# Kernel optimization log

Measured on AMD Instinct MI355X. Metric: run time of the kernel, lower is better.

## Reference

```python
import math
import jax, jax.numpy as jnp
import numpy as np

V, D_S, D_F, N_PASSES, N_HEADS, MAX_LEN, FFN_MULT = 32000, 128, 1024, 3, 4, 2048, 4
B, L = 2, 2048


def _ln(x, g, b, eps=1e-5):
    m = x.mean(-1, keepdims=True)
    v = ((x - m) ** 2).mean(-1, keepdims=True)
    return (x - m) * jax.lax.rsqrt(v + eps) * g + b


def _pairwise_kernel(q, mu, log_var, tau):
    # M[t,j] = q_t^2 . iv_j - 2 q_t . (mu_j*iv_j) + mu_j^2 . iv_j  -> [B,L,L]
    iv = jnp.exp(-log_var)
    mu_iv = mu * iv
    mu2_iv_sum = (mu * mu_iv).sum(-1)                      # [B,L]
    term1 = jnp.einsum('btd,bjd->btj', q * q, iv)
    term2 = jnp.einsum('btd,bjd->btj', q, mu_iv)
    mahal = term1 - 2.0 * term2 + mu2_iv_sum[:, None, :]
    return jnp.exp(-0.5 * mahal / tau)


def _causal_render(features, alpha, K, causal_mask):
    eff_a = alpha[:, None, :] * K * causal_mask            # [B,L,L]
    eff_a = jnp.clip(eff_a, 0.0, 1.0 - 1e-6)
    log_1ma = jnp.log1p(-eff_a)
    log_cum = jnp.cumsum(log_1ma, axis=-1)
    log_T = jnp.concatenate([jnp.zeros_like(log_cum[:, :, :1]), log_cum[:, :, :-1]], axis=-1)
    weights = eff_a * jnp.exp(log_T)
    return jnp.einsum('btj,bjf->btf', weights, features)


def setup_inputs() -> dict:
    key = jax.random.key(0)
    ks = jax.random.split(key, 16)
    P = N_PASSES - 1
    n = lambda k, shape, std: jax.random.normal(k, shape, dtype=jnp.float32) * std
    inp = {
        'token_ids': jax.random.randint(ks[0], (B, L), 0, V),
        'tok_mu': n(ks[1], (V, D_S), 0.02),
        'tok_log_var': jnp.zeros((V, D_S), jnp.float32),
        'tok_raw_alpha': jnp.zeros((V, 1), jnp.float32),
        'tok_features': n(ks[2], (V, D_F), 0.02),
        'pos_mu': n(ks[3], (MAX_LEN, D_S), 0.01),
        'log_tau': jnp.asarray(math.log(128.0), jnp.float32),
        'qp_w': jnp.broadcast_to(jnp.eye(D_S, dtype=jnp.float32), (N_HEADS, D_S, D_S)).copy(),
        'qp_b': jnp.zeros((N_HEADS, D_S), jnp.float32),
        'hp_w': n(ks[4], (D_F, N_HEADS * D_F), 0.02 / math.sqrt(2 * N_PASSES)),
        'hp_b': jnp.zeros((D_F,), jnp.float32),
        'mu_w': n(ks[5], (P, D_S, 2 * D_F), 0.02),
        'mu_b': jnp.zeros((P, D_S), jnp.float32),
        'ag_w': n(ks[6], (P, 1, 2 * D_F), 0.02),
        'ag_b': jnp.zeros((P, 1), jnp.float32),
        'ffn_ln_g': jnp.ones((P, 2 * D_F), jnp.float32),
        'ffn_ln_b': jnp.zeros((P, 2 * D_F), jnp.float32),
        'ffn_w1': n(ks[7], (P, FFN_MULT * D_F, 2 * D_F), 0.02),
        'ffn_b1': jnp.zeros((P, FFN_MULT * D_F), jnp.float32),
        'ffn_w2': n(ks[8], (P, D_F, FFN_MULT * D_F), 0.02),
        'ffn_b2': jnp.zeros((P, D_F), jnp.float32),
        'lnf_g': jnp.ones((D_F,), jnp.float32),
        'lnf_b': jnp.zeros((D_F,), jnp.float32),
        'lm_w': n(ks[9], (V, D_F), 0.02),
    }
    return inp


def reference(token_ids, tok_mu, tok_log_var, tok_raw_alpha, tok_features, pos_mu,
              log_tau, qp_w, qp_b, hp_w, hp_b, mu_w, mu_b, ag_w, ag_b,
              ffn_ln_g, ffn_ln_b, ffn_w1, ffn_b1, ffn_w2, ffn_b2, lnf_g, lnf_b, lm_w):
    Bsz, Ln = token_ids.shape
    mu = tok_mu[token_ids] + pos_mu[:Ln][None]             # [B,L,d_s]
    log_var = tok_log_var[token_ids]
    alpha = jax.nn.sigmoid(tok_raw_alpha[token_ids][..., 0])  # [B,L]
    features = tok_features[token_ids]                     # [B,L,d_f]
    tau = jnp.exp(log_tau)
    causal_mask = jnp.tril(jnp.ones((Ln, Ln), jnp.float32))
    meaning = None
    for p in range(N_PASSES):
        head_meanings = []
        for h in range(N_HEADS):
            q_h = jnp.einsum('bld,ed->ble', mu, qp_w[h]) + qp_b[h]
            K_h = _pairwise_kernel(q_h, mu, log_var, tau)
            head_meanings.append(_causal_render(features, alpha, K_h, causal_mask))
        meaning = jnp.einsum('blc,fc->blf', jnp.concatenate(head_meanings, -1), hp_w) + hp_b
        if p < N_PASSES - 1:
            ctx = jnp.concatenate([features, meaning], -1)  # [B,L,2*d_f]
            mu = mu + jnp.tanh(jnp.einsum('blc,dc->bld', ctx, mu_w[p]) + mu_b[p])
            alpha = alpha * jax.nn.sigmoid(jnp.einsum('blc,oc->blo', ctx, ag_w[p]) + ag_b[p])[..., 0]
            h1 = _ln(ctx, ffn_ln_g[p], ffn_ln_b[p])
            h2 = jax.nn.gelu(jnp.einsum('blc,hc->blh', h1, ffn_w1[p]) + ffn_b1[p], approximate=False)
            features = features + jnp.einsum('blh,fh->blf', h2, ffn_w2[p]) + ffn_b2[p]
    logits = jnp.einsum('blf,vf->blv', _ln(meaning, lnf_g, lnf_b), lm_w)
    return logits
```

## Files before the change

### kernel.cpp

```cpp
#include <hip/hip_runtime.h>

#define BB 2
#define LL 2048
#define DS 128
#define DF 1024
#define NH 4
#define NP 3
#define VV 32000
#define FFH 4096
#define CTXD 2048
#define RR (BB*LL)
#define NHDF (NH*DF)

enum { EPI_NONE=0, EPI_TANH=1, EPI_GELU=2, EPI_EXPM=3 };

#define BM 128
#define BN 128
#define BK 8

template<int EPI, bool BETA, bool BT, bool TRI>
__global__ __launch_bounds__(256) void gemm_f32(
    const float* __restrict__ A, int lda, long sA,
    const float* __restrict__ B, int ldb, long sB,
    float* __restrict__ C, int ldc, long sC,
    int M, int N, int K,
    const float* __restrict__ bias,
    const float* __restrict__ m2s, long sM2,
    const float* __restrict__ log_tau)
{
    __shared__ __align__(16) float As[BK][BM];
    __shared__ __align__(16) float Bs[BK][BN];
    int z = blockIdx.z;
    A += (long)z * sA; B += (long)z * sB; C += (long)z * sC;
    const float* m2p = (EPI == EPI_EXPM) ? (m2s + (long)z * sM2) : nullptr;

    int m0 = blockIdx.y * BM;
    int n0 = blockIdx.x * BN;
    int tid = threadIdx.x;
    int tx = tid & 15, ty = tid >> 4;

    float acc[8][8];
    #pragma unroll
    for (int i = 0; i < 8; i++)
        #pragma unroll
        for (int j = 0; j < 8; j++) acc[i][j] = 0.f;

    int kEnd = K;
    if (TRI) { int km = m0 + BM; kEnd = km < K ? km : K; }

    int arow = tid >> 1, akk = (tid & 1) * 4;
    for (int k0 = 0; k0 < kEnd; k0 += BK) {
        float4 av = *(const float4*)(A + (long)(m0 + arow) * lda + k0 + akk);
        As[akk+0][arow] = av.x; As[akk+1][arow] = av.y;
        As[akk+2][arow] = av.z; As[akk+3][arow] = av.w;
        if (BT) {
            float4 bv = *(const float4*)(B + (long)(n0 + arow) * ldb + k0 + akk);
            Bs[akk+0][arow] = bv.x; Bs[akk+1][arow] = bv.y;
            Bs[akk+2][arow] = bv.z; Bs[akk+3][arow] = bv.w;
        } else {
            int brow = tid >> 5, bcol = (tid & 31) * 4;
            float4 bv = *(const float4*)(B + (long)(k0 + brow) * ldb + n0 + bcol);
            *(float4*)&Bs[brow][bcol] = bv;
        }
        __syncthreads();
        #pragma unroll
        for (int kk = 0; kk < BK; kk++) {
            float a[8], b[8];
            *(float4*)&a[0] = *(const float4*)&As[kk][ty*8];
            *(float4*)&a[4] = *(const float4*)&As[kk][ty*8+4];
            *(float4*)&b[0] = *(const float4*)&Bs[kk][tx*8];
            *(float4*)&b[4] = *(const float4*)&Bs[kk][tx*8+4];
            #pragma unroll
            for (int i = 0; i < 8; i++)
                #pragma unroll
                for (int j = 0; j < 8; j++)
                    acc[i][j] = fmaf(a[i], b[j], acc[i][j]);
        }
        __syncthreads();
    }

    float scale = 0.f;
    if (EPI == EPI_EXPM) scale = -0.5f * expf(-log_tau[0]);

    #pragma unroll
    for (int i = 0; i < 8; i++) {
        int row = m0 + ty*8 + i;
        float* cp = C + (long)row * ldc + n0 + tx*8;
        float out[8];
        #pragma unroll
        for (int j = 0; j < 8; j++) {
            float v = acc[i][j];
            int col = n0 + tx*8 + j;
            if (EPI == EPI_EXPM) {
                v = expf(scale * (v + m2p[col]));
            } else {
                if (bias) v += bias[col];
                if (EPI == EPI_TANH) v = tanhf(v);
                else if (EPI == EPI_GELU) v = 0.5f*v*(1.f + erff(v*0.70710678118654752f));
            }
            out[j] = v;
        }
        if (BETA) {
            float4 c0 = *(const float4*)(cp);
            float4 c1 = *(const float4*)(cp + 4);
            out[0]+=c0.x; out[1]+=c0.y; out[2]+=c0.z; out[3]+=c0.w;
            out[4]+=c1.x; out[5]+=c1.y; out[6]+=c1.z; out[7]+=c1.w;
        }
        *(float4*)cp       = make_float4(out[0],out[1],out[2],out[3]);
        *(float4*)(cp + 4) = make_float4(out[4],out[5],out[6],out[7]);
    }
}

__global__ __launch_bounds__(256) void embed_kernel(
    const int* __restrict__ ids, const float* __restrict__ tok_mu,
    const float* __restrict__ tok_lv, const float* __restrict__ tok_ra,
    const float* __restrict__ tok_f, const float* __restrict__ pos_mu,
    float* __restrict__ mu, float* __restrict__ iv,
    float* __restrict__ alpha, float* __restrict__ feat)
{
    int r = blockIdx.x; int l = r % LL;
    int id = ids[r];
    int tid = threadIdx.x;
    for (int i = tid; i < DS; i += 256) {
        mu[(long)r*DS + i] = tok_mu[(long)id*DS + i] + pos_mu[(long)l*DS + i];
        iv[(long)r*DS + i] = expf(-tok_lv[(long)id*DS + i]);
    }
    for (int i = tid; i < DF; i += 256)
        feat[(long)r*DF + i] = tok_f[(long)id*DF + i];
    if (tid == 0) alpha[r] = 1.f/(1.f + expf(-tok_ra[id]));
}

__global__ __launch_bounds__(256) void alpha_kernel(
    const float* __restrict__ ctx, const float* __restrict__ agw,
    const float* __restrict__ agb, float* __restrict__ alpha)
{
    int r = blockIdx.x;
    const float* xr = ctx + (long)r*CTXD;
    __shared__ float red[256];
    int tid = threadIdx.x;
    float s = 0.f;
    for (int i = tid; i < CTXD; i += 256) s += xr[i]*agw[i];
    red[tid] = s; __syncthreads();
    for (int st = 128; st > 0; st >>= 1) { if (tid < st) red[tid] += red[tid+st]; __syncthreads(); }
    if (tid == 0) alpha[r] *= 1.f/(1.f + expf(-(red[0] + agb[0])));
}

__global__ __launch_bounds__(256) void ctx_kernel(
    const float* __restrict__ feat, const float* __restrict__ meaning, float* __restrict__ ctx)
{
    long i4 = (long)blockIdx.x * 256 + threadIdx.x;
    long r = i4 >> 9;
    long c4 = i4 & 511;
    const float4* src = (c4 < 256) ? (const float4*)(feat + r*DF) + c4
                                   : (const float4*)(meaning + r*DF) + (c4 - 256);
    ((float4*)ctx)[i4] = *src;
}

__global__ __launch_bounds__(128) void qbuild_kernel(
    const float* __restrict__ mu, const float* __restrict__ iv,
    float* __restrict__ Q, float* __restrict__ m2s)
{
    int r = blockIdx.x; int d = threadIdx.x;
    float ivd = iv[(long)r*DS + d];
    float m   = mu[(long)r*DS + d];
    Q[(long)r*256 + d]       = ivd;
    Q[(long)r*256 + 128 + d] = m * ivd;
    __shared__ float red[128];
    red[d] = m*m*ivd; __syncthreads();
    for (int s = 64; s > 0; s >>= 1) { if (d < s) red[d] += red[d+s]; __syncthreads(); }
    if (d == 0) m2s[r] = red[0];
}

__global__ __launch_bounds__(128) void pbuild_kernel(const float* __restrict__ q, float* __restrict__ P)
{
    int r = blockIdx.x; int d = threadIdx.x;
    float qv = q[(long)r*DS + d];
    P[(long)r*256 + d]       = qv*qv;
    P[(long)r*256 + 128 + d] = -2.f*qv;
}

__global__ __launch_bounds__(256) void scan_weights(float* __restrict__ Kmat, const float* __restrict__ alpha)
{
    int r = blockIdx.x;
    int b = r / LL, t = r % LL;
    float* row = Kmat + (long)r * LL;
    const float* al = alpha + (long)b * LL;
    int tid = threadIdx.x;
    int lane = tid & 63, wid = tid >> 6;
    __shared__ float wtot[4];
    float carry = 1.f;
    for (int j0 = 0; j0 < LL; j0 += 256) {
        int j = j0 + tid;
        if (j0 > t) { row[j] = 0.f; continue; }
        float eff = 0.f;
        if (j <= t) eff = fminf(al[j] * row[j], 1.f - 1e-6f);
        float om = 1.f - eff;
        float incl = om;
        #pragma unroll
        for (int d = 1; d < 64; d <<= 1) {
            float v = __shfl_up(incl, d);
            if (lane >= d) incl *= v;
        }
        if (lane == 63) wtot[wid] = incl;
        float excl = __shfl_up(incl, 1);
        if (lane == 0) excl = 1.f;
        __syncthreads();
        float wpre = carry;
        for (int w = 0; w < wid; w++) wpre *= wtot[w];
        row[j] = eff * wpre * excl;
        float tot = wtot[0]*wtot[1]*wtot[2]*wtot[3];
        __syncthreads();
        carry *= tot;
    }
}

template<int C>
__global__ __launch_bounds__(256) void ln_kernel(
    const float* __restrict__ x, const float* __restrict__ g,
    const float* __restrict__ b, float* __restrict__ y)
{
    int r = blockIdx.x;
    const float* xr = x + (long)r*C;
    __shared__ float xs[C];
    __shared__ float red[256];
    int tid = threadIdx.x;
    float s = 0.f;
    for (int i = tid; i < C; i += 256) { float v = xr[i]; xs[i] = v; s += v; }
    red[tid] = s; __syncthreads();
    for (int st = 128; st > 0; st >>= 1) { if (tid < st) red[tid] += red[tid+st]; __syncthreads(); }
    float mean = red[0] / C;
    __syncthreads();
    float s2 = 0.f;
    for (int i = tid; i < C; i += 256) { float d = xs[i]-mean; s2 += d*d; }
    red[tid] = s2; __syncthreads();
    for (int st = 128; st > 0; st >>= 1) { if (tid < st) red[tid] += red[tid+st]; __syncthreads(); }
    float rs = rsqrtf(red[0]/C + 1e-5f);
    for (int i = tid; i < C; i += 256) y[(long)r*C + i] = (xs[i]-mean)*rs*g[i] + b[i];
}

typedef __attribute__((ext_vector_type(8))) short bf8;
typedef __attribute__((ext_vector_type(4))) float f4;

__device__ __forceinline__ unsigned short bf16_rne(float x){
    unsigned u = __builtin_bit_cast(unsigned, x);
    u += 0x7FFFu + ((u >> 16) & 1u);
    return (unsigned short)(u >> 16);
}
__device__ __forceinline__ float bf16f(unsigned short h){
    unsigned u = ((unsigned)h) << 16;
    return __builtin_bit_cast(float, u);
}
__device__ __forceinline__ void split2(float x, unsigned short& h, unsigned short& l){
    h = bf16_rne(x);
    l = bf16_rne(x - bf16f(h));
}
__device__ __forceinline__ f4 mfma_b(bf8 a, bf8 b, f4 c){
    return __builtin_amdgcn_mfma_f32_16x16x32_bf16(a, b, c, 0, 0, 0);
}

template<int EPI, bool BETA, bool TRI, bool OSPLIT>
__global__ __launch_bounds__(256, 2) void gemm_mf(
    const unsigned short* __restrict__ Ah, const unsigned short* __restrict__ Al, int lda, long sA,
    const unsigned short* __restrict__ Bh, const unsigned short* __restrict__ Bl, int ldb, long sB,
    float* __restrict__ C, unsigned short* __restrict__ Ch, unsigned short* __restrict__ Cl,
    int ldc, long sC, int M, int N, int K,
    const float* __restrict__ bias, const float* __restrict__ m2s, long sM2,
    const float* __restrict__ log_tau)
{
    __shared__ __align__(16) unsigned short lds[4][4][128][8];

    int z = blockIdx.z;
    Ah += (long)z * sA; Al += (long)z * sA;
    Bh += (long)z * sB; Bl += (long)z * sB;
    if (OSPLIT) { Ch += (long)z * sC; Cl += (long)z * sC; }
    else        { C  += (long)z * sC; }
    const float* m2p = (EPI == EPI_EXPM) ? (m2s + (long)z * sM2) : nullptr;

    int m0 = blockIdx.y * 128, n0 = blockIdx.x * 128;
    int tid  = threadIdx.x;
    int lane = tid & 63, wave = tid >> 6;
    int wm = wave >> 1, wn = wave & 1;
    int kc = lane >> 4, lr = lane & 15;

    f4 acc[4][4];
    #pragma unroll
    for (int i = 0; i < 4; i++)
        #pragma unroll
        for (int j = 0; j < 4; j++)
            #pragma unroll
            for (int r = 0; r < 4; r++) acc[i][j][r] = 0.f;

    int kEnd = K;
    if (TRI) { int km = m0 + 128; kEnd = km < K ? km : K; }

    int s0 = tid, s1 = tid + 256;
    int row0 = s0 & 127, c0 = s0 >> 7;
    int row1 = s1 & 127, c1 = s1 >> 7;

    for (int kt = 0; kt < kEnd; kt += 32) {
        long a0 = (long)(m0 + row0) * lda + kt + c0 * 8;
        long a1 = (long)(m0 + row1) * lda + kt + c1 * 8;
        long b0 = (long)(n0 + row0) * ldb + kt + c0 * 8;
        long b1 = (long)(n0 + row1) * ldb + kt + c1 * 8;
        uint4 vah0 = *(const uint4*)(Ah + a0);
        uint4 vah1 = *(const uint4*)(Ah + a1);
        uint4 val0 = *(const uint4*)(Al + a0);
        uint4 val1 = *(const uint4*)(Al + a1);
        uint4 vbh0 = *(const uint4*)(Bh + b0);
        uint4 vbh1 = *(const uint4*)(Bh + b1);
        uint4 vbl0 = *(const uint4*)(Bl + b0);
        uint4 vbl1 = *(const uint4*)(Bl + b1);
        *(uint4*)&lds[0][c0][row0][0] = vah0;
        *(uint4*)&lds[0][c1][row1][0] = vah1;
        *(uint4*)&lds[1][c0][row0][0] = val0;
        *(uint4*)&lds[1][c1][row1][0] = val1;
        *(uint4*)&lds[2][c0][row0][0] = vbh0;
        *(uint4*)&lds[2][c1][row1][0] = vbh1;
        *(uint4*)&lds[3][c0][row0][0] = vbl0;
        *(uint4*)&lds[3][c1][row1][0] = vbl1;
        __syncthreads();

        bf8 ah[4], al4[4], bh4[4], bl4[4];
        #pragma unroll
        for (int i = 0; i < 4; i++) {
            ah[i]  = *(const bf8*)&lds[0][kc][wm*64 + i*16 + lr][0];
            al4[i] = *(const bf8*)&lds[1][kc][wm*64 + i*16 + lr][0];
            bh4[i] = *(const bf8*)&lds[2][kc][wn*64 + i*16 + lr][0];
            bl4[i] = *(const bf8*)&lds[3][kc][wn*64 + i*16 + lr][0];
        }
        #pragma unroll
        for (int i = 0; i < 4; i++)
            #pragma unroll
            for (int j = 0; j < 4; j++) {
                acc[i][j] = mfma_b(ah[i],  bh4[j], acc[i][j]);
                acc[i][j] = mfma_b(al4[i], bh4[j], acc[i][j]);
                acc[i][j] = mfma_b(ah[i],  bl4[j], acc[i][j]);
            }
        __syncthreads();
    }

    float scale = 0.f;
    if (EPI == EPI_EXPM) scale = -0.5f * expf(-log_tau[0]);
    int r0 = (lane >> 4) * 4;
    #pragma unroll
    for (int i = 0; i < 4; i++) {
        int rowb = m0 + wm*64 + i*16 + r0;
        #pragma unroll
        for (int j = 0; j < 4; j++) {
            int col = n0 + wn*64 + j*16 + lr;
            float bv = 0.f, m2v = 0.f;
            if (EPI == EPI_EXPM) m2v = m2p[col];
            else if (bias) bv = bias[col];
            #pragma unroll
            for (int r = 0; r < 4; r++) {
                long off = (long)(rowb + r) * ldc + col;
                float v = acc[i][j][r];
                if (EPI == EPI_EXPM) v = expf(scale * (v + m2v));
                else {
                    v += bv;
                    if (EPI == EPI_TANH) v = tanhf(v);
                    else if (EPI == EPI_GELU) v = 0.5f*v*(1.f + erff(v*0.70710678118654752f));
                }
                if (OSPLIT) {
                    unsigned short hh, llo; split2(v, hh, llo);
                    Ch[off] = hh; Cl[off] = llo;
                } else {
                    if (BETA) v += C[off];
                    C[off] = v;
                }
            }
        }
    }
}

__global__ __launch_bounds__(256) void split_kernel(
    const float* __restrict__ x, unsigned short* __restrict__ h, unsigned short* __restrict__ l)
{
    long i = (long)blockIdx.x * 256 + threadIdx.x;
    float4 v = ((const float4*)x)[i];
    ushort4 hv, lv;
    split2(v.x, hv.x, lv.x); split2(v.y, hv.y, lv.y);
    split2(v.z, hv.z, lv.z); split2(v.w, hv.w, lv.w);
    ((ushort4*)h)[i] = hv;
    ((ushort4*)l)[i] = lv;
}

__global__ __launch_bounds__(256) void tsplit_kernel(
    const float* __restrict__ x, unsigned short* __restrict__ th, unsigned short* __restrict__ tl)
{
    __shared__ float t[32][33];
    int bx = blockIdx.x, by = blockIdx.y;
    int tx = threadIdx.x & 31, ty = threadIdx.x >> 5;
    #pragma unroll
    for (int k = 0; k < 4; k++)
        t[ty + 8*k][tx] = x[(long)(by*32 + ty + 8*k)*DF + bx*32 + tx];
    __syncthreads();
    #pragma unroll
    for (int k = 0; k < 4; k++) {
        float v = t[tx][ty + 8*k];
        unsigned short hh, llo; split2(v, hh, llo);
        long o = (long)(bx*32 + ty + 8*k)*RR + by*32 + tx;
        th[o] = hh; tl[o] = llo;
    }
}

__global__ __launch_bounds__(128) void qbuild_mf(
    const float* __restrict__ mu, const float* __restrict__ iv,
    unsigned short* __restrict__ Qh, unsigned short* __restrict__ Ql,
    float* __restrict__ m2s)
{
    int r = blockIdx.x; int d = threadIdx.x;
    float ivd = iv[(long)r*DS + d];
    float m   = mu[(long)r*DS + d];
    unsigned short hh, llo;
    split2(ivd, hh, llo);
    Qh[(long)r*256 + d] = hh;        Ql[(long)r*256 + d] = llo;
    split2(m * ivd, hh, llo);
    Qh[(long)r*256 + 128 + d] = hh;  Ql[(long)r*256 + 128 + d] = llo;
    __shared__ float red[128];
    red[d] = m*m*ivd; __syncthreads();
    for (int s = 64; s > 0; s >>= 1) { if (d < s) red[d] += red[d+s]; __syncthreads(); }
    if (d == 0) m2s[r] = red[0];
}

__global__ __launch_bounds__(128) void pbuild_mf(
    const float* __restrict__ q,
    unsigned short* __restrict__ Ph, unsigned short* __restrict__ Pl)
{
    int r = blockIdx.x; int d = threadIdx.x;
    float qv = q[(long)r*DS + d];
    unsigned short hh, llo;
    split2(qv*qv, hh, llo);
    Ph[(long)r*256 + d] = hh;        Pl[(long)r*256 + d] = llo;
    split2(-2.f*qv, hh, llo);
    Ph[(long)r*256 + 128 + d] = hh;  Pl[(long)r*256 + 128 + d] = llo;
}

__global__ __launch_bounds__(256) void scan_weights_mf(
    const float* __restrict__ Kmat, const float* __restrict__ alpha,
    unsigned short* __restrict__ Wh, unsigned short* __restrict__ Wl)
{
    int r = blockIdx.x;
    int b = r / LL, t = r % LL;
    const float* row = Kmat + (long)r * LL;
    unsigned short* wh = Wh + (long)r * LL;
    unsigned short* wl = Wl + (long)r * LL;
    const float* al = alpha + (long)b * LL;
    int tid = threadIdx.x;
    int lane = tid & 63, wid = tid >> 6;
    __shared__ float wtot[4];
    float carry = 1.f;
    for (int j0 = 0; j0 < LL; j0 += 256) {
        int j = j0 + tid;
        if (j0 > t) { wh[j] = 0; wl[j] = 0; continue; }
        float eff = 0.f;
        if (j <= t) eff = fminf(al[j] * row[j], 1.f - 1e-6f);
        float om = 1.f - eff;
        float incl = om;
        #pragma unroll
        for (int d = 1; d < 64; d <<= 1) {
            float v = __shfl_up(incl, d);
            if (lane >= d) incl *= v;
        }
        if (lane == 63) wtot[wid] = incl;
        float excl = __shfl_up(incl, 1);
        if (lane == 0) excl = 1.f;
        __syncthreads();
        float wpre = carry;
        for (int w = 0; w < wid; w++) wpre *= wtot[w];
        float val = eff * wpre * excl;
        unsigned short hh, llo; split2(val, hh, llo);
        wh[j] = hh; wl[j] = llo;
        float tot = wtot[0]*wtot[1]*wtot[2]*wtot[3];
        __syncthreads();
        carry *= tot;
    }
}

template<int C>
__global__ __launch_bounds__(256) void ln_mf(
    const float* __restrict__ x, const float* __restrict__ g,
    const float* __restrict__ b, unsigned short* __restrict__ yh, unsigned short* __restrict__ yl)
{
    int r = blockIdx.x;
    const float* xr = x + (long)r*C;
    __shared__ float xs[C];
    __shared__ float red[256];
    int tid = threadIdx.x;
    float s = 0.f;
    for (int i = tid; i < C; i += 256) { float v = xr[i]; xs[i] = v; s += v; }
    red[tid] = s; __syncthreads();
    for (int st = 128; st > 0; st >>= 1) { if (tid < st) red[tid] += red[tid+st]; __syncthreads(); }
    float mean = red[0] / C;
    __syncthreads();
    float s2 = 0.f;
    for (int i = tid; i < C; i += 256) { float d = xs[i]-mean; s2 += d*d; }
    red[tid] = s2; __syncthreads();
    for (int st = 128; st > 0; st >>= 1) { if (tid < st) red[tid] += red[tid+st]; __syncthreads(); }
    float rs = rsqrtf(red[0]/C + 1e-5f);
    for (int i = tid; i < C; i += 256) {
        float v = (xs[i]-mean)*rs*g[i] + b[i];
        unsigned short hh, llo; split2(v, hh, llo);
        yh[(long)r*C + i] = hh; yl[(long)r*C + i] = llo;
    }
}

static void launch_legacy(void* const* d_in, void* d_out, void* d_ws, hipStream_t stream)
{
    const int*   token_ids = (const int*)d_in[0];
    const float* tok_mu  = (const float*)d_in[1];
    const float* tok_lv  = (const float*)d_in[2];
    const float* tok_ra  = (const float*)d_in[3];
    const float* tok_f   = (const float*)d_in[4];
    const float* pos_mu  = (const float*)d_in[5];
    const float* log_tau = (const float*)d_in[6];
    const float* qp_w = (const float*)d_in[7];
    const float* qp_b = (const float*)d_in[8];
    const float* hp_w = (const float*)d_in[9];
    const float* hp_b = (const float*)d_in[10];
    const float* mu_w = (const float*)d_in[11];
    const float* mu_b = (const float*)d_in[12];
    const float* ag_w = (const float*)d_in[13];
    const float* ag_b = (const float*)d_in[14];
    const float* ln_g = (const float*)d_in[15];
    const float* ln_b = (const float*)d_in[16];
    const float* w1 = (const float*)d_in[17];
    const float* b1 = (const float*)d_in[18];
    const float* w2 = (const float*)d_in[19];
    const float* b2 = (const float*)d_in[20];
    const float* lnf_g = (const float*)d_in[21];
    const float* lnf_b = (const float*)d_in[22];
    const float* lm_w  = (const float*)d_in[23];
    float* out = (float*)d_out;

    float* ws      = (float*)d_ws;
    float* mu      = ws;
    float* iv      = mu + 524288;
    float* alpha   = iv + 524288;
    float* m2s     = alpha + 4096;
    float* q       = m2s + 4096;
    float* P       = q + 524288;
    float* Q       = P + 1048576;
    float* feat    = Q + 1048576;
    float* meaning = feat + 4194304;
    float* head_m  = meaning + 4194304;
    float* ctx     = head_m + 4194304;
    float* Kbuf    = ctx + 8388608;
    float* h1  = Kbuf;
    float* h2  = head_m;
    float* lnm = head_m;

    const int R = BB * LL;

    embed_kernel<<<R, 256, 0, stream>>>(token_ids, tok_mu, tok_lv, tok_ra, tok_f, pos_mu,
                                        mu, iv, alpha, feat);

    for (int p = 0; p < NP; p++) {
        qbuild_kernel<<<R, 128, 0, stream>>>(mu, iv, Q, m2s);
        for (int h = 0; h < NH; h++) {
            dim3 g1(DS/BN, R/BM, 1);
            gemm_f32<EPI_NONE,false,true,false><<<g1,256,0,stream>>>(
                mu, DS, 0, qp_w + (long)h*DS*DS, DS, 0, q, DS, 0,
                R, DS, DS, qp_b + h*DS, nullptr, 0, nullptr);
            pbuild_kernel<<<R, 128, 0, stream>>>(q, P);
            dim3 g2(LL/BN, LL/BM, BB);
            gemm_f32<EPI_EXPM,false,true,false><<<g2,256,0,stream>>>(
                P, 256, (long)LL*256, Q, 256, (long)LL*256, Kbuf, LL, (long)LL*LL,
                LL, LL, 256, nullptr, m2s, LL, log_tau);
            scan_weights<<<R, 256, 0, stream>>>(Kbuf, alpha);
            dim3 g3(DF/BN, LL/BM, BB);
            gemm_f32<EPI_NONE,false,false,true><<<g3,256,0,stream>>>(
                Kbuf, LL, (long)LL*LL, feat, DF, (long)LL*DF, head_m, DF, (long)LL*DF,
                LL, DF, LL, nullptr, nullptr, 0, nullptr);
            dim3 g4(DF/BN, R/BM, 1);
            if (h == 0)
                gemm_f32<EPI_NONE,false,true,false><<<g4,256,0,stream>>>(
                    head_m, DF, 0, hp_w + (long)h*DF, NH*DF, 0, meaning, DF, 0,
                    R, DF, DF, hp_b, nullptr, 0, nullptr);
            else
                gemm_f32<EPI_NONE,true,true,false><<<g4,256,0,stream>>>(
                    head_m, DF, 0, hp_w + (long)h*DF, NH*DF, 0, meaning, DF, 0,
                    R, DF, DF, nullptr, nullptr, 0, nullptr);
        }
        if (p < NP - 1) {
            ctx_kernel<<<(R*CTXD/4)/256, 256, 0, stream>>>(feat, meaning, ctx);
            dim3 g5(DS/BN, R/BM, 1);
            gemm_f32<EPI_TANH,true,true,false><<<g5,256,0,stream>>>(
                ctx, CTXD, 0, mu_w + (long)p*DS*CTXD, CTXD, 0, mu, DS, 0,
                R, DS, CTXD, mu_b + p*DS, nullptr, 0, nullptr);
            alpha_kernel<<<R, 256, 0, stream>>>(ctx, ag_w + (long)p*CTXD, ag_b + p, alpha);
            ln_kernel<CTXD><<<R, 256, 0, stream>>>(ctx, ln_g + (long)p*CTXD, ln_b + (long)p*CTXD, h1);
            for (int c = 0; c < 4; c++) {
                long ro = (long)c * 1024;
                dim3 g6(FFH/BN, 1024/BM, 1);
                gemm_f32<EPI_GELU,false,true,false><<<g6,256,0,stream>>>(
                    h1 + ro*CTXD, CTXD, 0, w1 + (long)p*FFH*CTXD, CTXD, 0, h2, FFH, 0,
                    1024, FFH, CTXD, b1 + (long)p*FFH, nullptr, 0, nullptr);
                dim3 g7(DF/BN, 1024/BM, 1);
                gemm_f32<EPI_NONE,true,true,false><<<g7,256,0,stream>>>(
                    h2, FFH, 0, w2 + (long)p*DF*FFH, FFH, 0, feat + ro*DF, DF, 0,
                    1024, DF, FFH, b2 + (long)p*DF, nullptr, 0, nullptr);
            }
        }
    }

    ln_kernel<DF><<<R, 256, 0, stream>>>(meaning, lnf_g, lnf_b, lnm);
    dim3 g8(VV/BN, R/BM, 1);
    gemm_f32<EPI_NONE,false,true,false><<<g8,256,0,stream>>>(
        lnm, DF, 0, lm_w, DF, 0, out, VV, 0,
        R, VV, DF, nullptr, nullptr, 0, nullptr);
}

extern "C" void kernel_launch(void* const* d_in, const int* in_sizes, int n_in,
                              void* d_out, int out_size, void* d_ws, size_t ws_size,
                              hipStream_t stream)
{
    const size_t WS_NEED = 174096384;
    if (ws_size < WS_NEED) {
        launch_legacy(d_in, d_out, d_ws, stream);
        return;
    }

    const int*   token_ids = (const int*)d_in[0];
    const float* tok_mu  = (const float*)d_in[1];
    const float* tok_lv  = (const float*)d_in[2];
    const float* tok_ra  = (const float*)d_in[3];
    const float* tok_f   = (const float*)d_in[4];
    const float* pos_mu  = (const float*)d_in[5];
    const float* log_tau = (const float*)d_in[6];
    const float* qp_w = (const float*)d_in[7];
    const float* qp_b = (const float*)d_in[8];
    const float* hp_w = (const float*)d_in[9];
    const float* hp_b = (const float*)d_in[10];
    const float* mu_w = (const float*)d_in[11];
    const float* mu_b = (const float*)d_in[12];
    const float* ag_w = (const float*)d_in[13];
    const float* ag_b = (const float*)d_in[14];
    const float* ln_g = (const float*)d_in[15];
    const float* ln_b = (const float*)d_in[16];
    const float* w1 = (const float*)d_in[17];
    const float* b1 = (const float*)d_in[18];
    const float* w2 = (const float*)d_in[19];
    const float* b2 = (const float*)d_in[20];
    const float* lnf_g = (const float*)d_in[21];
    const float* lnf_b = (const float*)d_in[22];
    const float* lm_w  = (const float*)d_in[23];
    float* out = (float*)d_out;

    float* ws      = (float*)d_ws;
    float* mu      = ws;
    float* iv      = mu + 524288;
    float* alpha   = iv + 524288;
    float* m2s     = alpha + 4096;
    float* q       = m2s + 4096;
    float* feat    = q + 524288;
    float* meaning = feat + 4194304;
    float* ctxK    = meaning + 4194304;
    float* Kbuf = ctxK;
    float* ctx  = ctxK;

    unsigned short* pool = (unsigned short*)(ctxK + 8388608);
    unsigned short* featT_h = pool;
    unsigned short* featT_l = pool + 4194304;
    unsigned short* hpw_h   = pool + 8388608;
    unsigned short* hpw_l   = pool + 12582912;
    unsigned short* P_h     = pool + 16777216;
    unsigned short* P_l     = pool + 17825792;
    unsigned short* Q_h     = pool + 18874368;
    unsigned short* Q_l     = pool + 19922944;
    unsigned short* W_h     = pool + 20971520;
    unsigned short* W_l     = pool + 29360128;
    unsigned short* hm_h    = pool + 37748736;
    unsigned short* hm_l    = pool + 41943040;
    unsigned short* h1_h  = pool;
    unsigned short* h1_l  = pool + 4194304;
    unsigned short* w1s_h = pool + 8388608;
    unsigned short* w1s_l = pool + 16777216;
    unsigned short* h2_h  = pool + 25165824;
    unsigned short* h2_l  = pool + 33554432;
    unsigned short* w2s_h = pool + 41943040;
    unsigned short* w2s_l = pool + 46137344;
    unsigned short* lnm_h = pool;
    unsigned short* lnm_l = pool + 4194304;
    unsigned short* lmw_h = pool + 8388608;
    unsigned short* lmw_l = pool + 24772608;

    embed_kernel<<<RR, 256, 0, stream>>>(token_ids, tok_mu, tok_lv, tok_ra, tok_f, pos_mu,
                                         mu, iv, alpha, feat);

    for (int p = 0; p < NP; p++) {
        tsplit_kernel<<<dim3(DF/32, RR/32), 256, 0, stream>>>(feat, featT_h, featT_l);
        split_kernel<<<(DF*NHDF)/1024, 256, 0, stream>>>(hp_w, hpw_h, hpw_l);
        qbuild_mf<<<RR, 128, 0, stream>>>(mu, iv, Q_h, Q_l, m2s);
        for (int h = 0; h < NH; h++) {
            dim3 g1(DS/BN, RR/BM, 1);
            gemm_f32<EPI_NONE,false,true,false><<<g1,256,0,stream>>>(
                mu, DS, 0, qp_w + (long)h*DS*DS, DS, 0, q, DS, 0,
                RR, DS, DS, qp_b + h*DS, nullptr, 0, nullptr);
            pbuild_mf<<<RR, 128, 0, stream>>>(q, P_h, P_l);
            dim3 g2(LL/128, LL/128, BB);
            gemm_mf<EPI_EXPM,false,false,false><<<g2,256,0,stream>>>(
                P_h, P_l, 256, (long)LL*256, Q_h, Q_l, 256, (long)LL*256,
                Kbuf, nullptr, nullptr, LL, (long)LL*LL,
                LL, LL, 256, nullptr, m2s, LL, log_tau);
            scan_weights_mf<<<RR, 256, 0, stream>>>(Kbuf, alpha, W_h, W_l);
            dim3 g3(DF/128, LL/128, BB);
            gemm_mf<EPI_NONE,false,true,true><<<g3,256,0,stream>>>(
                W_h, W_l, LL, (long)LL*LL, featT_h, featT_l, RR, (long)LL,
                nullptr, hm_h, hm_l, DF, (long)LL*DF,
                LL, DF, LL, nullptr, nullptr, 0, nullptr);
            dim3 g4(DF/128, RR/128, 1);
            if (h == 0)
                gemm_mf<EPI_NONE,false,false,false><<<g4,256,0,stream>>>(
                    hm_h, hm_l, DF, 0, hpw_h + (long)h*DF, hpw_l + (long)h*DF, NHDF, 0,
                    meaning, nullptr, nullptr, DF, 0,
                    RR, DF, DF, hp_b, nullptr, 0, nullptr);
            else
                gemm_mf<EPI_NONE,true,false,false><<<g4,256,0,stream>>>(
                    hm_h, hm_l, DF, 0, hpw_h + (long)h*DF, hpw_l + (long)h*DF, NHDF, 0,
                    meaning, nullptr, nullptr, DF, 0,
                    RR, DF, DF, nullptr, nullptr, 0, nullptr);
        }
        if (p < NP - 1) {
            ctx_kernel<<<(RR*CTXD/4)/256, 256, 0, stream>>>(feat, meaning, ctx);
            dim3 g5(DS/BN, RR/BM, 1);
            gemm_f32<EPI_TANH,true,true,false><<<g5,256,0,stream>>>(
                ctx, CTXD, 0, mu_w + (long)p*DS*CTXD, CTXD, 0, mu, DS, 0,
                RR, DS, CTXD, mu_b + p*DS, nullptr, 0, nullptr);
            alpha_kernel<<<RR, 256, 0, stream>>>(ctx, ag_w + (long)p*CTXD, ag_b + p, alpha);
            split_kernel<<<(FFH*CTXD)/1024, 256, 0, stream>>>(w1 + (long)p*FFH*CTXD, w1s_h, w1s_l);
            split_kernel<<<(DF*FFH)/1024, 256, 0, stream>>>(w2 + (long)p*DF*FFH, w2s_h, w2s_l);
            for (int c = 0; c < 2; c++) {
                long ro = (long)c * 2048;
                ln_mf<CTXD><<<2048, 256, 0, stream>>>(
                    ctx + ro*CTXD, ln_g + (long)p*CTXD, ln_b + (long)p*CTXD, h1_h, h1_l);
                dim3 g6(FFH/128, 2048/128, 1);
                gemm_mf<EPI_GELU,false,false,true><<<g6,256,0,stream>>>(
                    h1_h, h1_l, CTXD, 0, w1s_h, w1s_l, CTXD, 0,
                    nullptr, h2_h, h2_l, FFH, 0,
                    2048, FFH, CTXD, b1 + (long)p*FFH, nullptr, 0, nullptr);
                dim3 g7(DF/128, 2048/128, 1);
                gemm_mf<EPI_NONE,true,false,false><<<g7,256,0,stream>>>(
                    h2_h, h2_l, FFH, 0, w2s_h, w2s_l, FFH, 0,
                    feat + ro*DF, nullptr, nullptr, DF, 0,
                    2048, DF, FFH, b2 + (long)p*DF, nullptr, 0, nullptr);
            }
        }
    }

    ln_mf<DF><<<RR, 256, 0, stream>>>(meaning, lnf_g, lnf_b, lnm_h, lnm_l);
    for (int c = 0; c < 2; c++) {
        split_kernel<<<(16000*DF)/1024, 256, 0, stream>>>(lm_w + (long)c*16000*DF, lmw_h, lmw_l);
        dim3 g8(16000/128, RR/128, 1);
        gemm_mf<EPI_NONE,false,false,false><<<g8,256,0,stream>>>(
            lnm_h, lnm_l, DF, 0, lmw_h, lmw_l, DF, 0,
            out + (long)c*16000, nullptr, nullptr, VV, 0,
            RR, 16000, DF, nullptr, nullptr, 0, nullptr);
    }
}
```

Baseline: 7.476 ms.

## Use direct global-to-LDS loads and XCD-aware block remapping in split-bf16 GEMM

Replaces register-staged global loads followed by LDS stores with 16-byte global_load_lds intrinsics, so tiles go straight into shared memory without passing through VGPRs. Also remaps workgroup IDs so that consecutive tiles (walking M-major within a column of N) land on the same XCD, which should improve L2 reuse across the chiplets. Risks: global_load_lds writes each lane's 16 bytes to LDS at a wave-uniform base plus lane offset, so per-lane LDS addresses may not match the intended layout. There is also no explicit vmcnt wait before the barrier, which could give wrong results.

```diff
diff --git a/kernel.cpp b/kernel.cpp
--- a/kernel.cpp
+++ b/kernel.cpp
@@ -257,6 +257,11 @@
 __device__ __forceinline__ f4 mfma_b(bf8 a, bf8 b, f4 c){
     return __builtin_amdgcn_mfma_f32_16x16x32_bf16(a, b, c, 0, 0, 0);
 }
+__device__ __forceinline__ void gload16(const unsigned short* g, unsigned short* l){
+    __builtin_amdgcn_global_load_lds(
+        (const __attribute__((address_space(1))) unsigned int*)g,
+        (__attribute__((address_space(3))) unsigned int*)l, 16, 0, 0);
+}
 
 template<int EPI, bool BETA, bool TRI, bool OSPLIT>
 __global__ __launch_bounds__(256, 2) void gemm_mf(
@@ -276,9 +281,18 @@
     else        { C  += (long)z * sC; }
     const float* m2p = (EPI == EPI_EXPM) ? (m2s + (long)z * sM2) : nullptr;
 
-    int m0 = blockIdx.y * 128, n0 = blockIdx.x * 128;
+    int gx = gridDim.x, gy = gridDim.y;
+    int nwg = gx * gy;
+    int orig = blockIdx.y * gx + blockIdx.x;
+    int qq = nwg >> 3, rmod = nwg & 7;
+    int xcd = orig & 7, idx = orig >> 3;
+    int wgid = (xcd < rmod ? xcd * (qq + 1) : rmod * (qq + 1) + (xcd - rmod) * qq) + idx;
+    int m0 = (wgid % gy) * 128;
+    int n0 = (wgid / gy) * 128;
+
     int tid  = threadIdx.x;
-    int lane = tid & 63, wave = tid >> 6;
+    int lane = tid & 63;
+    int wave = tid >> 6;
     int wm = wave >> 1, wn = wave & 1;
     int kc = lane >> 4, lr = lane & 15;
 
@@ -302,22 +316,14 @@
         long a1 = (long)(m0 + row1) * lda + kt + c1 * 8;
         long b0 = (long)(n0 + row0) * ldb + kt + c0 * 8;
         long b1 = (long)(n0 + row1) * ldb + kt + c1 * 8;
-        uint4 vah0 = *(const uint4*)(Ah + a0);
-        uint4 vah1 = *(const uint4*)(Ah + a1);
-        uint4 val0 = *(const uint4*)(Al + a0);
-        uint4 val1 = *(const uint4*)(Al + a1);
-        uint4 vbh0 = *(const uint4*)(Bh + b0);
-        uint4 vbh1 = *(const uint4*)(Bh + b1);
-        uint4 vbl0 = *(const uint4*)(Bl + b0);
-        uint4 vbl1 = *(const uint4*)(Bl + b1);
-        *(uint4*)&lds[0][c0][row0][0] = vah0;
-        *(uint4*)&lds[0][c1][row1][0] = vah1;
-        *(uint4*)&lds[1][c0][row0][0] = val0;
-        *(uint4*)&lds[1][c1][row1][0] = val1;
-        *(uint4*)&lds[2][c0][row0][0] = vbh0;
-        *(uint4*)&lds[2][c1][row1][0] = vbh1;
-        *(uint4*)&lds[3][c0][row0][0] = vbl0;
-        *(uint4*)&lds[3][c1][row1][0] = vbl1;
+        gload16(Ah + a0, &lds[0][c0][row0][0]);
+        gload16(Ah + a1, &lds[0][c1][row1][0]);
+        gload16(Al + a0, &lds[1][c0][row0][0]);
+        gload16(Al + a1, &lds[1][c1][row1][0]);
+        gload16(Bh + b0, &lds[2][c0][row0][0]);
+        gload16(Bh + b1, &lds[2][c1][row1][0]);
+        gload16(Bl + b0, &lds[3][c0][row0][0]);
+        gload16(Bl + b1, &lds[3][c1][row1][0]);
         __syncthreads();
 
         bf8 ah[4], al4[4], bh4[4], bl4[4];
```

Result: faster. 7.153 ms (-4.3%).
